# Performance work log

Hardware: AMD Instinct MI355X
Metric: run time of the kernel (lower is better)

## Reference

```python
import jax, jax.numpy as jnp
import numpy as np

SEQ = 2048
DIM = 512
HEADS = 8
DH = DIM // HEADS
EPS = float(np.finfo(np.float32).eps)
NEG = float(np.finfo(np.float32).max)


def _pos_encoding(seq, dim):
    idx = jnp.arange(seq, dtype=jnp.float32)
    div = 1.0 / (10000.0 ** (jnp.arange(0, dim, 2, dtype=jnp.float32) / dim) + EPS)
    ang = idx[:, None] * div[None, :]  # [S, dim/2]
    pos = jnp.zeros((seq, dim), dtype=jnp.float32)
    pos = pos.at[:, 0::2].set(jnp.sin(ang)).at[:, 1::2].set(jnp.cos(ang))
    return pos[None]  # [1, S, D]


def _rmsnorm(x, gain, bias):
    d = x.shape[-1]
    scale = jnp.linalg.norm(x, axis=-1, keepdims=True) * (d ** -0.5)
    return x / (scale + EPS) * gain + bias


def setup_inputs() -> dict:
    key = jax.random.key(0)
    ks = jax.random.split(key, 12)
    s = 0.02
    return {
        "x": jax.random.normal(ks[0], (4, SEQ, DIM), dtype=jnp.float32),
        "norm1_g": jnp.ones((DIM,), jnp.float32),
        "norm1_b": jnp.zeros((DIM,), jnp.float32),
        "wq": jax.random.normal(ks[1], (DIM, DIM), jnp.float32) * s,
        "wk": jax.random.normal(ks[2], (DIM, DIM), jnp.float32) * s,
        "wv": jax.random.normal(ks[3], (DIM, DIM), jnp.float32) * s,
        "wo": jax.random.normal(ks[4], (DIM, DIM), jnp.float32) * s,
        "norm2_g": jnp.ones((DIM,), jnp.float32),
        "norm2_b": jnp.zeros((DIM,), jnp.float32),
        "ff_w1": jax.random.normal(ks[5], (DIM, DIM), jnp.float32) * s,
        "ff_b1": jnp.zeros((DIM,), jnp.float32),
        "ffn_g": jnp.ones((DIM,), jnp.float32),
        "ffn_b": jnp.zeros((DIM,), jnp.float32),
        "sw_w": jax.random.normal(ks[6], (2 * DIM, DIM), jnp.float32) * s,
        "sw_b": jnp.zeros((2 * DIM,), jnp.float32),
        "ff_w2": jax.random.normal(ks[7], (DIM, DIM), jnp.float32) * s,
        "ff_b2": jnp.zeros((DIM,), jnp.float32),
    }


def _block(x, norm1_g, norm1_b, wq, wk, wv, wo, norm2_g, norm2_b,
           ff_w1, ff_b1, ffn_g, ffn_b, sw_w, sw_b, ff_w2, ff_b2):
    B = x.shape[0]
    x = x + _pos_encoding(SEQ, DIM)

    # --- multi-head attention on RMSNorm(x) ---
    h = _rmsnorm(x, norm1_g, norm1_b)
    q = (h @ wq.T).reshape(B, SEQ, HEADS, DH).transpose(0, 2, 1, 3)  # [B,H,S,Dh]
    k = (h @ wk.T).reshape(B, SEQ, HEADS, DH).transpose(0, 2, 1, 3)
    v = (h @ wv.T).reshape(B, SEQ, HEADS, DH).transpose(0, 2, 1, 3)
    scores = jnp.einsum("bhqd,bhkd->bhqk", q, k)  # materialized [B,H,S,S]
    causal_mask = jnp.triu(jnp.ones((SEQ, SEQ), dtype=bool), k=1)
    scores = jnp.where(causal_mask[None, None], -NEG, scores)
    # NOTE: original scales by dim_k**-0.5 = dim_emb**-0.5 (not head dim)
    attn = jax.nn.softmax(scores * (DIM ** -0.5), axis=-1)
    o = jnp.einsum("bhqk,bhkd->bhqd", attn, v)
    o = o.transpose(0, 2, 1, 3).reshape(B, SEQ, DIM) @ wo.T
    x = x + o

    # --- feed-forward: Linear -> RMSNorm -> SwiGLU -> Linear ---
    h = _rmsnorm(x, norm2_g, norm2_b)
    h = h @ ff_w1.T + ff_b1
    h = _rmsnorm(h, ffn_g, ffn_b)
    u = h @ sw_w.T + sw_b  # [B,S,2*DIM]
    h = jax.nn.silu(u[..., :DIM]) + u[..., DIM:]
    h = h @ ff_w2.T + ff_b2
    return x + h


def reference(x, norm1_g, norm1_b, wq, wk, wv, wo, norm2_g, norm2_b,
              ff_w1, ff_b1, ffn_g, ffn_b, sw_w, sw_b, ff_w2, ff_b2):
    return _block(x, norm1_g, norm1_b, wq, wk, wv, wo, norm2_g, norm2_b,
                  ff_w1, ff_b1, ffn_g, ffn_b, sw_w, sw_b, ff_w2, ff_b2)
```

## Files before the change

kernel.cpp:

```cpp
#include <hip/hip_runtime.h>
#include <hip/hip_bf16.h>
#include <cstdint>
#include <cstddef>

typedef __bf16 bf16;
typedef __bf16 bf16x4_t __attribute__((ext_vector_type(4)));
typedef __bf16 bf16x8_t __attribute__((ext_vector_type(8)));
typedef float f32x4 __attribute__((ext_vector_type(4)));
typedef float f32x16 __attribute__((ext_vector_type(16)));

#define DEV_INLINE __device__ __forceinline__

constexpr int SEQ = 2048, DIM = 512, HEADS = 8, DH = 64;
constexpr int ROWS = 4 * SEQ;
constexpr float EPSF = 1.1920928955078125e-07f;
constexpr float RSQRT_DIM = 0.04419417382415922f;
constexpr float LOG2E = 1.44269504088896f;

DEV_INLINE void load_lds16(const void* g, void* l) {
  __builtin_amdgcn_global_load_lds(
      (const __attribute__((address_space(1))) void*)g,
      (__attribute__((address_space(3))) void*)l,
      16, 0, 0);
}

DEV_INLINE unsigned int packbf(float a, float b) {
  union { unsigned int u; bf16 h[2]; } z;
  z.h[0] = (bf16)a;
  z.h[1] = (bf16)b;
  return z.u;
}

DEV_INLINE void permswap(unsigned int& a, unsigned int& b) {
  asm volatile("v_permlane32_swap_b32 %0, %1" : "+v"(a), "+v"(b));
}

__global__ __launch_bounds__(256) void cvt_all_k(
    const float* __restrict__ wq, const float* __restrict__ wk,
    const float* __restrict__ wv, const float* __restrict__ wo,
    const float* __restrict__ w1, const float* __restrict__ sww,
    const float* __restrict__ w2, bf16* __restrict__ dst) {
  const int i = blockIdx.x * 256 + threadIdx.x;
  const float* src;
  int local;
  if (i < 196608)      { src = (i < 65536) ? wq : (i < 131072) ? wk : wv; local = i & 65535; }
  else if (i < 262144) { src = wo;  local = i - 196608; }
  else if (i < 327680) { src = w1;  local = i - 262144; }
  else if (i < 458752) { src = sww; local = i - 327680; }
  else                 { src = w2;  local = i - 458752; }
  float4 f = reinterpret_cast<const float4*>(src)[local];
  bf16x4_t o;
  o[0] = (bf16)f.x; o[1] = (bf16)f.y; o[2] = (bf16)f.z; o[3] = (bf16)f.w;
  reinterpret_cast<bf16x4_t*>(dst)[i] = o;
}

template <bool ADDPOS>
__global__ __launch_bounds__(256) void rmsnorm_k(const float* __restrict__ in,
                                                 const float* __restrict__ gain,
                                                 const float* __restrict__ bias,
                                                 float* __restrict__ outF,
                                                 bf16* __restrict__ outB) {
  const int sub = threadIdx.x >> 7;
  const int row = blockIdx.x * 2 + sub;
  const int t = threadIdx.x & 127;
  const float* rp = in + (size_t)row * DIM;
  float4 v = reinterpret_cast<const float4*>(rp)[t];
  if constexpr (ADDPOS) {
    const int s = row & (SEQ - 1);
    const float e0 = (float)(4 * t) * (1.0f / (float)DIM);
    const float e1 = (float)(4 * t + 2) * (1.0f / (float)DIM);
    const float d0 = 1.0f / (powf(10000.0f, e0) + EPSF);
    const float d1 = 1.0f / (powf(10000.0f, e1) + EPSF);
    const float a0 = (float)s * d0, a1 = (float)s * d1;
    v.x += sinf(a0); v.y += cosf(a0);
    v.z += sinf(a1); v.w += cosf(a1);
  }
  float ss = v.x * v.x + v.y * v.y + v.z * v.z + v.w * v.w;
#pragma unroll
  for (int off = 32; off > 0; off >>= 1) ss += __shfl_down(ss, off, 64);
  __shared__ float red[4];
  const int wv = threadIdx.x >> 6;
  if ((threadIdx.x & 63) == 0) red[wv] = ss;
  __syncthreads();
  const float total = red[sub * 2] + red[sub * 2 + 1];
  const float scale = sqrtf(total) * RSQRT_DIM;
  const float inv = 1.0f / (scale + EPSF);
  if constexpr (ADDPOS)
    reinterpret_cast<float4*>(outF + (size_t)row * DIM)[t] = v;
  const float4 g = reinterpret_cast<const float4*>(gain)[t];
  const float4 bb = reinterpret_cast<const float4*>(bias)[t];
  bf16x4_t o;
  o[0] = (bf16)(v.x * inv * g.x + bb.x);
  o[1] = (bf16)(v.y * inv * g.y + bb.y);
  o[2] = (bf16)(v.z * inv * g.z + bb.z);
  o[3] = (bf16)(v.w * inv * g.w + bb.w);
  reinterpret_cast<bf16x4_t*>(outB + (size_t)row * DIM)[t] = o;
}

enum { MODE_QKV = 0, MODE_RES = 1, MODE_BIAS = 2, MODE_SWIGLU2 = 3, MODE_RESBIAS = 4 };

template <int MODE>
__global__ __launch_bounds__(256) void gemm_bt_k(
    const bf16* __restrict__ A, const bf16* __restrict__ Bt,
    const float* __restrict__ bias, const float* __restrict__ res,
    float* __restrict__ outF, bf16* __restrict__ outB,
    bf16* __restrict__ oq, bf16* __restrict__ okk, bf16* __restrict__ ovT) {
  constexpr int BELEMS = (MODE == MODE_SWIGLU2) ? 4096 : 2048;
  __shared__ __align__(16) bf16 sA[3][128 * 32];
  __shared__ __align__(16) bf16 sB[3][BELEMS];
  const int tid = threadIdx.x;
  const int wave = tid >> 6, lane = tid & 63;
  const int m0 = blockIdx.x * 128, n0 = blockIdx.y * 64;
  const int wm = wave >> 1, wn = wave & 1;
  const int lr = lane & 15, lk = (lane >> 4) * 8;

  const f32x4 fzero = {0.f, 0.f, 0.f, 0.f};
  f32x4 acc[4][2], acc2[4][2];
#pragma unroll
  for (int i = 0; i < 4; ++i)
#pragma unroll
    for (int j = 0; j < 2; ++j) { acc[i][j] = fzero; acc2[i][j] = fzero; }

  const int off0 = wave * 1024 + lane * 16;
  const int rowS = off0 >> 6, colb = off0 & 63;

  auto stage = [&](int buf, int kt) {
    const int k0 = kt * 32;
    load_lds16((const char*)A + ((size_t)(m0 + rowS) * 512 + k0) * 2 + colb,
               (char*)&sA[buf][0] + off0);
    load_lds16((const char*)A + ((size_t)(m0 + 64 + rowS) * 512 + k0) * 2 + colb,
               (char*)&sA[buf][0] + 4096 + off0);
    load_lds16((const char*)Bt + ((size_t)(n0 + rowS) * 512 + k0) * 2 + colb,
               (char*)&sB[buf][0] + off0);
    if constexpr (MODE == MODE_SWIGLU2)
      load_lds16((const char*)Bt + ((size_t)(512 + n0 + rowS) * 512 + k0) * 2 + colb,
                 (char*)&sB[buf][0] + 4096 + off0);
  };

  stage(0, 0);
  stage(1, 1);
  if constexpr (MODE == MODE_SWIGLU2)
    asm volatile("s_waitcnt vmcnt(4)\ns_barrier" ::: "memory");
  else
    asm volatile("s_waitcnt vmcnt(3)\ns_barrier" ::: "memory");

#pragma unroll
  for (int kt = 0; kt < 16; ++kt) {
    const int cur = kt % 3;
    if (kt + 2 < 16) stage((kt + 2) % 3, kt + 2);
    bf16x8_t af[4], bfr[2], bfr2[2];
#pragma unroll
    for (int mf = 0; mf < 4; ++mf)
      af[mf] = *(const bf16x8_t*)(&sA[cur][0] + (wm * 64 + mf * 16 + lr) * 32 + lk);
#pragma unroll
    for (int nf = 0; nf < 2; ++nf)
      bfr[nf] = *(const bf16x8_t*)(&sB[cur][0] + (wn * 32 + nf * 16 + lr) * 32 + lk);
    if constexpr (MODE == MODE_SWIGLU2) {
#pragma unroll
      for (int nf = 0; nf < 2; ++nf)
        bfr2[nf] = *(const bf16x8_t*)(&sB[cur][0] + 2048 + (wn * 32 + nf * 16 + lr) * 32 + lk);
    }
    asm volatile("s_waitcnt lgkmcnt(0)" ::: "memory");
#pragma unroll
    for (int mf = 0; mf < 4; ++mf)
#pragma unroll
      for (int nf = 0; nf < 2; ++nf) {
        acc[mf][nf] = __builtin_amdgcn_mfma_f32_16x16x32_bf16(af[mf], bfr[nf],
                                                              acc[mf][nf], 0, 0, 0);
        if constexpr (MODE == MODE_SWIGLU2)
          acc2[mf][nf] = __builtin_amdgcn_mfma_f32_16x16x32_bf16(af[mf], bfr2[nf],
                                                                 acc2[mf][nf], 0, 0, 0);
      }
    if (kt < 14) {
      if constexpr (MODE == MODE_SWIGLU2)
        asm volatile("s_waitcnt vmcnt(4)\ns_barrier" ::: "memory");
      else
        asm volatile("s_waitcnt vmcnt(3)\ns_barrier" ::: "memory");
    } else if (kt < 15) {
      asm volatile("s_waitcnt vmcnt(0)\ns_barrier" ::: "memory");
    }
  }

  if constexpr (MODE == MODE_QKV) {
    const int which = n0 >> 9;
    const int h = (n0 >> 6) & 7;
    const int b = m0 >> 11;
    const int s0tok = m0 & 2047;
    bf16* st = &sA[0][0];
    const int rb = wm * 64 + (lane >> 4) * 4;
    const int cb = wn * 32 + lr;
    __syncthreads();
    if (which < 2) {
#pragma unroll
      for (int mf = 0; mf < 4; ++mf)
#pragma unroll
        for (int nf = 0; nf < 2; ++nf)
#pragma unroll
          for (int rg = 0; rg < 4; ++rg) {
            float v = acc[mf][nf][rg];
            if (which == 0) v *= RSQRT_DIM * LOG2E;
            st[(rb + mf * 16 + rg) * 72 + cb + nf * 16] = (bf16)v;
          }
      __syncthreads();
      bf16* dst = which == 0 ? oq : okk;
#pragma unroll
      for (int j = 0; j < 4; ++j) {
        const int flat = j * 4096 + tid * 16;
        const int row = flat >> 7, offb = flat & 127;
        bf16x8_t vv = *(const bf16x8_t*)(st + row * 72 + offb / 2);
        const size_t addr =
            ((size_t)((b * HEADS + h) * SEQ + s0tok + row)) * DH + offb / 2;
        *(bf16x8_t*)(dst + addr) = vv;
      }
    } else {
#pragma unroll
      for (int mf = 0; mf < 4; ++mf)
#pragma unroll
        for (int nf = 0; nf < 2; ++nf)
#pragma unroll
          for (int rg = 0; rg < 4; ++rg)
            st[(cb + nf * 16) * 136 + rb + mf * 16 + rg] = (bf16)acc[mf][nf][rg];
      __syncthreads();
#pragma unroll
      for (int j = 0; j < 4; ++j) {
        const int flat = j * 4096 + tid * 16;
        const int row = flat >> 8, offb = flat & 255;
        bf16x8_t vv = *(const bf16x8_t*)(st + row * 136 + offb / 2);
        const size_t addr =
            ((size_t)((b * HEADS + h) * DH + row)) * SEQ + s0tok + offb / 2;
        *(bf16x8_t*)(ovT + addr) = vv;
      }
    }
    return;
  }

  const int rbase = m0 + wm * 64 + (lane >> 4) * 4;
  const int cbase = n0 + wn * 32 + lr;
#pragma unroll
  for (int mf = 0; mf < 4; ++mf) {
#pragma unroll
    for (int nf = 0; nf < 2; ++nf) {
      const int c = cbase + nf * 16;
#pragma unroll
      for (int rg = 0; rg < 4; ++rg) {
        const int r = rbase + mf * 16 + rg;
        float v = acc[mf][nf][rg];
        if constexpr (MODE == MODE_RES) {
          const size_t idx = (size_t)r * 512 + c;
          outF[idx] = res[idx] + v;
        } else if constexpr (MODE == MODE_BIAS) {
          const size_t idx = (size_t)r * 512 + c;
          outF[idx] = v + bias[c];
        } else if constexpr (MODE == MODE_SWIGLU2) {
          const size_t idx = (size_t)r * 512 + c;
          const float u1 = v + bias[c];
          const float u2 = acc2[mf][nf][rg] + bias[512 + c];
          const float sig = 1.0f / (1.0f + __expf(-u1));
          outB[idx] = (bf16)(u1 * sig + u2);
        } else {
          const size_t idx = (size_t)r * 512 + c;
          outF[idx] = res[idx] + v + bias[c];
        }
      }
    }
  }
}

__global__ __launch_bounds__(256)
__attribute__((amdgpu_waves_per_eu(2, 2)))
void attn_k(const bf16* __restrict__ Q,
            const bf16* __restrict__ K,
            const bf16* __restrict__ VT,
            bf16* __restrict__ O) {
  const int tid = threadIdx.x;
  const int wave = tid >> 6, lane = tid & 63;
  const int lq = lane & 31, hi = lane >> 5;

  const int wg = blockIdx.x;
  const int xcd = wg & 7;
  const int bh = xcd * 4 + ((wg >> 3) & 3);
  const int qi = 15 - (wg >> 5);
  const int qb = qi * 128;
  const int qw = qb + wave * 32;
  const int NT = qi * 2 + 2;
  const int nkt = qi * 2 + 1 + (wave >> 1);

  const char* Kg = (const char*)(K + (size_t)bh * SEQ * DH);
  const char* Vg = (const char*)(VT + (size_t)bh * DH * SEQ);
  const bf16* Qp = Q + (size_t)bh * SEQ * DH;

  __shared__ __align__(16) bf16 smem[4][4096];

  bf16x8_t qf[4];
  {
    const bf16* qp = Qp + (size_t)(qw + lq) * DH + 8 * hi;
    qf[0] = *(const bf16x8_t*)(qp);
    qf[1] = *(const bf16x8_t*)(qp + 16);
    qf[2] = *(const bf16x8_t*)(qp + 32);
    qf[3] = *(const bf16x8_t*)(qp + 48);
  }

  const int slot = lane & 7, rsub = lane >> 3;
  const int sgoff = (slot * 16) ^ (rsub << 4);

  auto stage = [&](int buf, int kt) {
#pragma unroll
    for (int c = 0; c < 2; ++c) {
      const int row = c * 32 + wave * 8 + rsub;
      const int ldsb = c * 4096 + wave * 1024 + lane * 16;
      load_lds16(Kg + (size_t)(kt * 64 + row) * 128 + sgoff,
                 (char*)&smem[buf][0] + ldsb);
      load_lds16(Vg + (size_t)row * 4096 + (size_t)kt * 128 + sgoff,
                 (char*)&smem[2 + buf][0] + ldsb);
    }
  };

  stage(0, 0);
  asm volatile("s_waitcnt vmcnt(0)" ::: "memory");
  __builtin_amdgcn_s_barrier();

  f32x16 oa0, oa1;
#pragma unroll
  for (int r = 0; r < 16; ++r) { oa0[r] = 0.f; oa1[r] = 0.f; }
  float lsum = 0.f;
  const int xorv = (lq & 7) << 4;

  union U8 { unsigned int u[4]; bf16x8_t v; };

  for (int kt = 0; kt < NT; ++kt) {
    const int buf = kt & 1;
    if (kt + 1 < NT) stage(buf ^ 1, kt + 1);
    if (kt < nkt) {
      const char* kb = (const char*)&smem[buf][0];
      const char* vb = (const char*)&smem[2 + buf][0];

      f32x16 s0, s1;
#pragma unroll
      for (int r = 0; r < 16; ++r) { s0[r] = 0.f; s1[r] = 0.f; }
      __builtin_amdgcn_s_setprio(1);
#pragma unroll
      for (int s = 0; s < 4; ++s) {
        const int bo = (32 * s + 16 * hi) ^ xorv;
        s0 = __builtin_amdgcn_mfma_f32_32x32x16_bf16(
            *(const bf16x8_t*)(kb + lq * 128 + bo), qf[s], s0, 0, 0, 0);
        s1 = __builtin_amdgcn_mfma_f32_32x32x16_bf16(
            *(const bf16x8_t*)(kb + (32 + lq) * 128 + bo), qf[s], s1, 0, 0, 0);
      }
      __builtin_amdgcn_s_setprio(0);

      if (kt == nkt - 1) {
        const int qg = qw + lq;
#pragma unroll
        for (int r = 0; r < 16; ++r) {
          const int kl = kt * 64 + (r & 3) + 8 * (r >> 2) + 4 * hi;
          if (kl > qg) s0[r] = -3.0e38f;
          if (kl + 32 > qg) s1[r] = -3.0e38f;
        }
      }

#pragma unroll
      for (int r = 0; r < 16; ++r) {
        const float a = exp2f(s0[r]); s0[r] = a; lsum += a;
        const float b = exp2f(s1[r]); s1[r] = b; lsum += b;
      }

      U8 p00, p01, p10, p11;
      {
        unsigned int x0, x1, y0, y1;
        x0 = packbf(s0[0], s0[1]);  x1 = packbf(s0[4], s0[5]);
        y0 = packbf(s0[2], s0[3]);  y1 = packbf(s0[6], s0[7]);
        permswap(x0, x1); permswap(y0, y1);
        p00.u[0] = x0; p00.u[2] = x1; p00.u[1] = y0; p00.u[3] = y1;
        x0 = packbf(s0[8], s0[9]);   x1 = packbf(s0[12], s0[13]);
        y0 = packbf(s0[10], s0[11]); y1 = packbf(s0[14], s0[15]);
        permswap(x0, x1); permswap(y0, y1);
        p01.u[0] = x0; p01.u[2] = x1; p01.u[1] = y0; p01.u[3] = y1;
        x0 = packbf(s1[0], s1[1]);  x1 = packbf(s1[4], s1[5]);
        y0 = packbf(s1[2], s1[3]);  y1 = packbf(s1[6], s1[7]);
        permswap(x0, x1); permswap(y0, y1);
        p10.u[0] = x0; p10.u[2] = x1; p10.u[1] = y0; p10.u[3] = y1;
        x0 = packbf(s1[8], s1[9]);   x1 = packbf(s1[12], s1[13]);
        y0 = packbf(s1[10], s1[11]); y1 = packbf(s1[14], s1[15]);
        permswap(x0, x1); permswap(y0, y1);
        p11.u[0] = x0; p11.u[2] = x1; p11.u[1] = y0; p11.u[3] = y1;
      }

      __builtin_amdgcn_s_setprio(1);
      {
        const int b0 = (16 * hi) ^ xorv;
        const int b1 = (32 + 16 * hi) ^ xorv;
        const int b2 = (64 + 16 * hi) ^ xorv;
        const int b3 = (96 + 16 * hi) ^ xorv;
        oa0 = __builtin_amdgcn_mfma_f32_32x32x16_bf16(
            *(const bf16x8_t*)(vb + lq * 128 + b0), p00.v, oa0, 0, 0, 0);
        oa0 = __builtin_amdgcn_mfma_f32_32x32x16_bf16(
            *(const bf16x8_t*)(vb + lq * 128 + b1), p01.v, oa0, 0, 0, 0);
        oa0 = __builtin_amdgcn_mfma_f32_32x32x16_bf16(
            *(const bf16x8_t*)(vb + lq * 128 + b2), p10.v, oa0, 0, 0, 0);
        oa0 = __builtin_amdgcn_mfma_f32_32x32x16_bf16(
            *(const bf16x8_t*)(vb + lq * 128 + b3), p11.v, oa0, 0, 0, 0);
        oa1 = __builtin_amdgcn_mfma_f32_32x32x16_bf16(
            *(const bf16x8_t*)(vb + (32 + lq) * 128 + b0), p00.v, oa1, 0, 0, 0);
        oa1 = __builtin_amdgcn_mfma_f32_32x32x16_bf16(
            *(const bf16x8_t*)(vb + (32 + lq) * 128 + b1), p01.v, oa1, 0, 0, 0);
        oa1 = __builtin_amdgcn_mfma_f32_32x32x16_bf16(
            *(const bf16x8_t*)(vb + (32 + lq) * 128 + b2), p10.v, oa1, 0, 0, 0);
        oa1 = __builtin_amdgcn_mfma_f32_32x32x16_bf16(
            *(const bf16x8_t*)(vb + (32 + lq) * 128 + b3), p11.v, oa1, 0, 0, 0);
      }
      __builtin_amdgcn_s_setprio(0);
    }
    asm volatile("s_waitcnt vmcnt(0)" ::: "memory");
    __builtin_amdgcn_s_barrier();
  }

  const float lrun = lsum + __shfl_xor(lsum, 32);
  const float inv = 1.0f / lrun;
  bf16* ol = &smem[0][0] + wave * 2560;
#pragma unroll
  for (int t4 = 0; t4 < 4; ++t4) {
    const int d0 = 8 * t4 + 4 * hi;
    *(unsigned int*)(ol + lq * 80 + d0)          = packbf(oa0[4 * t4] * inv, oa0[4 * t4 + 1] * inv);
    *(unsigned int*)(ol + lq * 80 + d0 + 2)      = packbf(oa0[4 * t4 + 2] * inv, oa0[4 * t4 + 3] * inv);
    *(unsigned int*)(ol + lq * 80 + 32 + d0)     = packbf(oa1[4 * t4] * inv, oa1[4 * t4 + 1] * inv);
    *(unsigned int*)(ol + lq * 80 + 32 + d0 + 2) = packbf(oa1[4 * t4 + 2] * inv, oa1[4 * t4 + 3] * inv);
  }
  const int b = bh >> 3, h = bh & 7;
#pragma unroll
  for (int ps = 0; ps < 4; ++ps) {
    const int flat = ps * 1024 + lane * 16;
    const int qr = flat >> 7, off = flat & 127;
    bf16x8_t vv = *(const bf16x8_t*)((const char*)ol + qr * 160 + off);
    *(bf16x8_t*)(O + ((size_t)(b * SEQ + qw + qr)) * DIM + h * 64 + off / 2) = vv;
  }
}

extern "C" void kernel_launch(void* const* d_in, const int* in_sizes, int n_in,
                              void* d_out, int out_size, void* d_ws, size_t ws_size,
                              hipStream_t stream) {
  const float* x   = (const float*)d_in[0];
  const float* n1g = (const float*)d_in[1];
  const float* n1b = (const float*)d_in[2];
  const float* wq  = (const float*)d_in[3];
  const float* wk  = (const float*)d_in[4];
  const float* wv  = (const float*)d_in[5];
  const float* wo  = (const float*)d_in[6];
  const float* n2g = (const float*)d_in[7];
  const float* n2b = (const float*)d_in[8];
  const float* w1  = (const float*)d_in[9];
  const float* b1  = (const float*)d_in[10];
  const float* ffg = (const float*)d_in[11];
  const float* ffb = (const float*)d_in[12];
  const float* sww = (const float*)d_in[13];
  const float* swb = (const float*)d_in[14];
  const float* w2  = (const float*)d_in[15];
  const float* b2  = (const float*)d_in[16];
  float* out = (float*)d_out;

  char* ws = (char*)d_ws;
  float* x1 = (float*)(ws + 0);
  float* x2 = (float*)(ws + 16777216);
  bf16* hbuf   = (bf16*)(ws + 33554432);
  bf16* qbuf   = (bf16*)(ws + 41943040);
  bf16* kbuf   = (bf16*)(ws + 50331648);
  bf16* vtbuf  = (bf16*)(ws + 58720256);
  bf16* obuf   = (bf16*)(ws + 67108864);
  bf16* wbase  = (bf16*)(ws + 75497472);
  bf16* wqkv_b = wbase;
  bf16* wo_b   = wbase + 786432;
  bf16* w1_b   = wbase + 1048576;
  bf16* sw_b16 = wbase + 1310720;
  bf16* w2_b   = wbase + 1835008;

  cvt_all_k<<<2048, 256, 0, stream>>>(wq, wk, wv, wo, w1, sww, w2, wbase);

  rmsnorm_k<true><<<ROWS / 2, 256, 0, stream>>>(x, n1g, n1b, x1, hbuf);

  gemm_bt_k<MODE_QKV><<<dim3(64, 24), 256, 0, stream>>>(
      hbuf, wqkv_b, nullptr, nullptr, nullptr, nullptr, qbuf, kbuf, vtbuf);

  attn_k<<<512, 256, 0, stream>>>(qbuf, kbuf, vtbuf, obuf);

  gemm_bt_k<MODE_RES><<<dim3(64, 8), 256, 0, stream>>>(
      obuf, wo_b, nullptr, x1, x2, nullptr, nullptr, nullptr, nullptr);

  rmsnorm_k<false><<<ROWS / 2, 256, 0, stream>>>(x2, n2g, n2b, nullptr, hbuf);

  gemm_bt_k<MODE_BIAS><<<dim3(64, 8), 256, 0, stream>>>(
      hbuf, w1_b, b1, nullptr, x1, nullptr, nullptr, nullptr, nullptr);

  rmsnorm_k<false><<<ROWS / 2, 256, 0, stream>>>(x1, ffg, ffb, nullptr, hbuf);

  gemm_bt_k<MODE_SWIGLU2><<<dim3(64, 8), 256, 0, stream>>>(
      hbuf, sw_b16, swb, nullptr, nullptr, qbuf, nullptr, nullptr, nullptr);

  gemm_bt_k<MODE_RESBIAS><<<dim3(64, 8), 256, 0, stream>>>(
      qbuf, w2_b, b2, x2, out, nullptr, nullptr, nullptr, nullptr);
}
```

Baseline: 158.9 us.

## Deepen GEMM and attention prefetch pipelines and reorder attention tile schedule

The GEMM kernel moves from three to four LDS stages with a prefetch distance of three tiles, and its vmcnt waits are adjusted to match. The attention kernel moves from double to triple buffering with a prefetch distance of two and waits only on the older loads. It also changes the query-block order for work-groups past 256 so they run shortest tiles first, and relaxes the waves_per_eu cap. The aim is to hide more global-load latency and balance causal work, at the cost of more LDS per block, which may lower occupancy.

```diff
diff --git a/kernel.cpp b/kernel.cpp
--- a/kernel.cpp
+++ b/kernel.cpp
@@ -106,8 +106,8 @@
     float* __restrict__ outF, bf16* __restrict__ outB,
     bf16* __restrict__ oq, bf16* __restrict__ okk, bf16* __restrict__ ovT) {
   constexpr int BELEMS = (MODE == MODE_SWIGLU2) ? 4096 : 2048;
-  __shared__ __align__(16) bf16 sA[3][128 * 32];
-  __shared__ __align__(16) bf16 sB[3][BELEMS];
+  __shared__ __align__(16) bf16 sA[4][128 * 32];
+  __shared__ __align__(16) bf16 sB[4][BELEMS];
   const int tid = threadIdx.x;
   const int wave = tid >> 6, lane = tid & 63;
   const int m0 = blockIdx.x * 128, n0 = blockIdx.y * 64;
@@ -139,15 +139,16 @@
 
   stage(0, 0);
   stage(1, 1);
+  stage(2, 2);
   if constexpr (MODE == MODE_SWIGLU2)
-    asm volatile("s_waitcnt vmcnt(4)\ns_barrier" ::: "memory");
+    asm volatile("s_waitcnt vmcnt(8)\ns_barrier" ::: "memory");
   else
-    asm volatile("s_waitcnt vmcnt(3)\ns_barrier" ::: "memory");
+    asm volatile("s_waitcnt vmcnt(6)\ns_barrier" ::: "memory");
 
 #pragma unroll
   for (int kt = 0; kt < 16; ++kt) {
-    const int cur = kt % 3;
-    if (kt + 2 < 16) stage((kt + 2) % 3, kt + 2);
+    const int cur = kt & 3;
+    if (kt + 3 < 16) stage((kt + 3) & 3, kt + 3);
     bf16x8_t af[4], bfr[2], bfr2[2];
 #pragma unroll
     for (int mf = 0; mf < 4; ++mf)
@@ -171,12 +172,17 @@
           acc2[mf][nf] = __builtin_amdgcn_mfma_f32_16x16x32_bf16(af[mf], bfr2[nf],
                                                                  acc2[mf][nf], 0, 0, 0);
       }
-    if (kt < 14) {
+    if (kt < 13) {
+      if constexpr (MODE == MODE_SWIGLU2)
+        asm volatile("s_waitcnt vmcnt(8)\ns_barrier" ::: "memory");
+      else
+        asm volatile("s_waitcnt vmcnt(6)\ns_barrier" ::: "memory");
+    } else if (kt == 13) {
       if constexpr (MODE == MODE_SWIGLU2)
         asm volatile("s_waitcnt vmcnt(4)\ns_barrier" ::: "memory");
       else
         asm volatile("s_waitcnt vmcnt(3)\ns_barrier" ::: "memory");
-    } else if (kt < 15) {
+    } else if (kt == 14) {
       asm volatile("s_waitcnt vmcnt(0)\ns_barrier" ::: "memory");
     }
   }
@@ -267,7 +273,7 @@
 }
 
 __global__ __launch_bounds__(256)
-__attribute__((amdgpu_waves_per_eu(2, 2)))
+__attribute__((amdgpu_waves_per_eu(2)))
 void attn_k(const bf16* __restrict__ Q,
             const bf16* __restrict__ K,
             const bf16* __restrict__ VT,
@@ -279,7 +285,7 @@
   const int wg = blockIdx.x;
   const int xcd = wg & 7;
   const int bh = xcd * 4 + ((wg >> 3) & 3);
-  const int qi = 15 - (wg >> 5);
+  const int qi = (wg < 256) ? (15 - (wg >> 5)) : ((wg - 256) >> 5);
   const int qb = qi * 128;
   const int qw = qb + wave * 32;
   const int NT = qi * 2 + 2;
@@ -289,7 +295,7 @@
   const char* Vg = (const char*)(VT + (size_t)bh * DH * SEQ);
   const bf16* Qp = Q + (size_t)bh * SEQ * DH;
 
-  __shared__ __align__(16) bf16 smem[4][4096];
+  __shared__ __align__(16) bf16 smem[6][4096];
 
   bf16x8_t qf[4];
   {
@@ -311,13 +317,13 @@
       load_lds16(Kg + (size_t)(kt * 64 + row) * 128 + sgoff,
                  (char*)&smem[buf][0] + ldsb);
       load_lds16(Vg + (size_t)row * 4096 + (size_t)kt * 128 + sgoff,
-                 (char*)&smem[2 + buf][0] + ldsb);
+                 (char*)&smem[3 + buf][0] + ldsb);
     }
   };
 
   stage(0, 0);
-  asm volatile("s_waitcnt vmcnt(0)" ::: "memory");
-  __builtin_amdgcn_s_barrier();
+  stage(1, 1);
+  asm volatile("s_waitcnt vmcnt(4)\ns_barrier" ::: "memory");
 
   f32x16 oa0, oa1;
 #pragma unroll
@@ -328,11 +334,11 @@
   union U8 { unsigned int u[4]; bf16x8_t v; };
 
   for (int kt = 0; kt < NT; ++kt) {
-    const int buf = kt & 1;
-    if (kt + 1 < NT) stage(buf ^ 1, kt + 1);
+    const int buf = kt % 3;
+    if (kt + 2 < NT) stage((kt + 2) % 3, kt + 2);
     if (kt < nkt) {
       const char* kb = (const char*)&smem[buf][0];
-      const char* vb = (const char*)&smem[2 + buf][0];
+      const char* vb = (const char*)&smem[3 + buf][0];
 
       f32x16 s0, s1;
 #pragma unroll
@@ -410,8 +416,10 @@
       }
       __builtin_amdgcn_s_setprio(0);
     }
-    asm volatile("s_waitcnt vmcnt(0)" ::: "memory");
-    __builtin_amdgcn_s_barrier();
+    if (kt + 2 < NT)
+      asm volatile("s_waitcnt vmcnt(4)\ns_barrier" ::: "memory");
+    else
+      asm volatile("s_waitcnt vmcnt(0)\ns_barrier" ::: "memory");
   }
 
   const float lrun = lsum + __shfl_xor(lsum, 32);
```

New measurement: 158.4 us. About the same (-0.3%).
